# Kernel tuning notes

Hardware: AMD Instinct MI355X
Metric: run time of the kernel (lower is better)

The kernel has to match this reference:

```python
import jax, jax.numpy as jnp
import numpy as np

TOPK = 3  # matches init_kwargs topk


def setup_inputs() -> dict:
    key = jax.random.key(0)
    k1, k2, k3 = jax.random.split(key, 3)
    B, N, D, E, L = 256, 1024, 1024, 8, 1000
    features = jax.random.normal(k1, (B, N, D), dtype=jnp.float32)
    gate_w = jax.random.normal(k2, (D, E), dtype=jnp.float32) * (1.0 / np.sqrt(D))
    gate_b = jnp.zeros((E,), dtype=jnp.float32)
    cls_w = jax.random.normal(k3, (E, L, D), dtype=jnp.float32) * (1.0 / np.sqrt(D))
    cls_b = jnp.zeros((E, L), dtype=jnp.float32)
    return {"features": features, "gate_w": gate_w, "gate_b": gate_b,
            "cls_w": cls_w, "cls_b": cls_b}


def reference(features, gate_w, gate_b, cls_w, cls_b):
    # features: [B, N, D]; gate_w: [D, E]; cls_w: [E, L, D]
    B = features.shape[0]
    E = cls_w.shape[0]
    gate_score = features @ gate_w + gate_b                      # [B, N, E]
    gate_prob = jax.nn.softmax(gate_score.transpose(0, 2, 1), axis=-1)  # [B, E, N] softmax over tokens
    top_v, top_i = jax.lax.top_k(gate_prob, TOPK)                # [B, E, K]
    # gather top-k token features per expert -> [B, E, K, D]
    gathered = features[jnp.arange(B)[:, None, None], top_i]
    comb_w = jax.nn.softmax(top_v, axis=-1)                      # [B, E, K]
    # per-expert linear: [B, E, K, L]
    logits = jnp.einsum('bekd,eld->bekl', gathered, cls_w) + cls_b[None, :, None, :]
    # weighted sum over K, then mean over experts -> [B, L]
    out = jnp.einsum('bekl,bek->bl', logits, comb_w) / E
    return out
```

## Files before the change

kernel.cpp:

```cpp
#include <hip/hip_runtime.h>
#include <hip/hip_bf16.h>
#include <cfloat>

#define B_ 256
#define N_ 1024
#define D_ 1024
#define E_ 8
#define L_ 1000

typedef float f32x4 __attribute__((ext_vector_type(4)));
typedef short bf16x8 __attribute__((ext_vector_type(8)));

__device__ inline unsigned short f2bf(float f) {
  unsigned u = __builtin_bit_cast(unsigned, f);
  u += 0x7fffu + ((u >> 16) & 1u);
  return (unsigned short)(u >> 16);
}

__global__ __launch_bounds__(256) void k_gate(const float* __restrict__ feat,
                                              const float* __restrict__ gate_w,
                                              float* __restrict__ scores) {
  __shared__ float gwT[E_ * D_];
  const int t = threadIdx.x;
#pragma unroll
  for (int j = 0; j < 32; ++j) {
    int idx = j * 256 + t;
    int e = idx & 7, d = idx >> 3;
    gwT[e * D_ + d] = gate_w[idx];
  }
  __syncthreads();

  const int wave = t >> 6, lane = t & 63;
  const long rowBase = ((long)blockIdx.x * 4 + wave) * 8;
  const float* fbase = feat + rowBase * D_;

  float acc[64];
#pragma unroll
  for (int j = 0; j < 64; ++j) acc[j] = 0.f;

#pragma unroll
  for (int it = 0; it < 4; ++it) {
    const int d0 = it * 256 + lane * 4;
    float4 f[8];
#pragma unroll
    for (int r = 0; r < 8; ++r) f[r] = *(const float4*)(fbase + r * D_ + d0);
#pragma unroll
    for (int e = 0; e < 8; ++e) {
      const float4 g = *(const float4*)(&gwT[e * D_ + d0]);
#pragma unroll
      for (int r = 0; r < 8; ++r) {
        acc[r * 8 + e] = fmaf(f[r].x, g.x,
                         fmaf(f[r].y, g.y,
                         fmaf(f[r].z, g.z,
                         fmaf(f[r].w, g.w, acc[r * 8 + e]))));
      }
    }
  }

#pragma unroll
  for (int s = 0; s < 6; ++s) {
    const int m = 1 << s;
    const int half = 32 >> s;
    const bool up = (lane & m) != 0;
#pragma unroll
    for (int j = 0; j < half; ++j) {
      float keep = up ? acc[j + half] : acc[j];
      float send = up ? acc[j] : acc[j + half];
      float recv = __shfl_xor(send, m, 64);
      acc[j] = keep + recv;
    }
  }
  const int idx = ((lane & 1) << 5) | ((lane & 2) << 3) | ((lane & 4) << 1) |
                  ((lane & 8) >> 1) | ((lane & 16) >> 3) | ((lane & 32) >> 5);
  scores[rowBase * 8 + idx] = acc[0];
}

__global__ __launch_bounds__(256) void k_topk(const float* __restrict__ scores,
                                              int* __restrict__ top_i,
                                              float* __restrict__ comb) {
  const int t = threadIdx.x, wave = t >> 6, lane = t & 63;
  const int pair = blockIdx.x * 4 + wave;
  const int b = pair >> 3, e = pair & 7;
  const float* s = scores + (long)b * N_ * E_ + e;

  float v[16];
#pragma unroll
  for (int j = 0; j < 16; ++j) v[j] = s[(j * 64 + lane) * E_];

  float M[3];
  int I[3];
  float Z = 0.f;
#pragma unroll
  for (int k = 0; k < 3; ++k) {
    float lm = -FLT_MAX;
    int ln = 0x7fffffff;
#pragma unroll
    for (int j = 0; j < 16; ++j) {
      if (v[j] > lm) { lm = v[j]; ln = j * 64 + lane; }
    }
#pragma unroll
    for (int s2 = 1; s2 < 64; s2 <<= 1) {
      float om = __shfl_xor(lm, s2, 64);
      int on = __shfl_xor(ln, s2, 64);
      if (om > lm || (om == lm && on < ln)) { lm = om; ln = on; }
    }
    M[k] = lm;
    I[k] = ln;
    if (k == 0) {
      float se = 0.f;
#pragma unroll
      for (int j = 0; j < 16; ++j) se += expf(v[j] - lm);
#pragma unroll
      for (int s2 = 1; s2 < 64; s2 <<= 1) se += __shfl_xor(se, s2, 64);
      Z = se;
    }
    const int slot = ln >> 6, owner = ln & 63;
#pragma unroll
    for (int j = 0; j < 16; ++j)
      if (j == slot && owner == lane) v[j] = -FLT_MAX;
  }

  if (lane == 0) {
    const float p0 = 1.f / Z;
    const float p1 = expf(M[1] - M[0]) / Z;
    const float p2 = expf(M[2] - M[0]) / Z;
    const float c1 = expf(p1 - p0);
    const float c2 = expf(p2 - p0);
    const float den = 1.f + c1 + c2;
    top_i[pair * 3 + 0] = I[0];
    top_i[pair * 3 + 1] = I[1];
    top_i[pair * 3 + 2] = I[2];
    comb[pair * 3 + 0] = 1.f / den;
    comb[pair * 3 + 1] = c1 / den;
    comb[pair * 3 + 2] = c2 / den;
  }
}

__global__ __launch_bounds__(256) void k_gather(const float* __restrict__ feat,
                                                const int* __restrict__ top_i,
                                                const float* __restrict__ comb,
                                                unsigned short* __restrict__ wf) {
  const int pair = blockIdx.x;
  const int b = pair >> 3;
  const int i0 = top_i[pair * 3 + 0];
  const int i1 = top_i[pair * 3 + 1];
  const int i2 = top_i[pair * 3 + 2];
  const float c0 = comb[pair * 3 + 0];
  const float c1 = comb[pair * 3 + 1];
  const float c2 = comb[pair * 3 + 2];
  const float* f = feat + (long)b * N_ * D_;
  const int d = threadIdx.x * 4;
  const float4 x = *(const float4*)(f + (long)i0 * D_ + d);
  const float4 y = *(const float4*)(f + (long)i1 * D_ + d);
  const float4 z = *(const float4*)(f + (long)i2 * D_ + d);
  ushort4 o;
  o.x = f2bf(c0 * x.x + c1 * y.x + c2 * z.x);
  o.y = f2bf(c0 * x.y + c1 * y.y + c2 * z.y);
  o.z = f2bf(c0 * x.z + c1 * y.z + c2 * z.z);
  o.w = f2bf(c0 * x.w + c1 * y.w + c2 * z.w);
  *(ushort4*)(wf + (long)pair * D_ + d) = o;
}

__global__ __launch_bounds__(256) void k_cls(const unsigned short* __restrict__ wf,
                                             const float* __restrict__ cls_w,
                                             float* __restrict__ part) {
  __shared__ uint4 Ag[2][128 * 8];
  __shared__ uint4 Bg[2][64 * 8];

  const int bx = blockIdx.x;
  const int e = bx >> 5, bt = (bx >> 4) & 1, lt = bx & 15;
  const int m0 = bt * 128, l0 = lt * 64;
  const int t = threadIdx.x;
  const int w = t >> 6, lane = t & 63;
  const int wm = w >> 1, wn = w & 1;

  const int arow = t >> 1, ah = t & 1;
  const int brow = t >> 2, bq = t & 3;
  const int lg = (l0 + brow < L_) ? (l0 + brow) : (L_ - 1);
  const unsigned short* agp = wf + ((size_t)(m0 + arow) * E_ + e) * D_ + ah * 32;
  const float* bgp = cls_w + ((size_t)e * L_ + lg) * D_ + bq * 16;

  uint4 areg[4];
  float4 breg[4];

  auto load_regs = [&](int step) {
    const int d0 = step * 64;
#pragma unroll
    for (int j = 0; j < 4; ++j)
      areg[j] = *(const uint4*)(agp + d0 + j * 8);
#pragma unroll
    for (int j = 0; j < 4; ++j)
      breg[j] = *(const float4*)(bgp + d0 + j * 4);
  };

  auto write_lds = [&](int c) {
#pragma unroll
    for (int j = 0; j < 4; ++j)
      Ag[c][arow * 8 + ((ah * 4 + j) ^ (arow & 7))] = areg[j];
#pragma unroll
    for (int j = 0; j < 2; ++j) {
      const float4 x = breg[j * 2], y = breg[j * 2 + 1];
      uint4 p;
      p.x = (unsigned)f2bf(x.x) | ((unsigned)f2bf(x.y) << 16);
      p.y = (unsigned)f2bf(x.z) | ((unsigned)f2bf(x.w) << 16);
      p.z = (unsigned)f2bf(y.x) | ((unsigned)f2bf(y.y) << 16);
      p.w = (unsigned)f2bf(y.z) | ((unsigned)f2bf(y.w) << 16);
      Bg[c][brow * 8 + ((bq * 2 + j) ^ (brow & 7))] = p;
    }
  };

  f32x4 acc[4][2];
#pragma unroll
  for (int m = 0; m < 4; ++m)
#pragma unroll
    for (int n = 0; n < 2; ++n) acc[m][n] = (f32x4){0.f, 0.f, 0.f, 0.f};

  const int l15 = lane & 15, lhi = lane >> 4, l7 = lane & 7;

  load_regs(0);
  for (int step = 0; step < 16; ++step) {
    const int c = step & 1;
    write_lds(c);
    if (step < 15) load_regs(step + 1);
    __syncthreads();
#pragma unroll
    for (int ks = 0; ks < 2; ++ks) {
      bf16x8 a[4], b[2];
#pragma unroll
      for (int m = 0; m < 4; ++m) {
        const int row = wm * 64 + m * 16 + l15;
        a[m] = __builtin_bit_cast(bf16x8,
                 Ag[c][row * 8 + ((ks * 4 + lhi) ^ l7)]);
      }
#pragma unroll
      for (int n = 0; n < 2; ++n) {
        const int row = wn * 32 + n * 16 + l15;
        b[n] = __builtin_bit_cast(bf16x8,
                 Bg[c][row * 8 + ((ks * 4 + lhi) ^ l7)]);
      }
#pragma unroll
      for (int m = 0; m < 4; ++m)
#pragma unroll
        for (int n = 0; n < 2; ++n)
          acc[m][n] = __builtin_amdgcn_mfma_f32_16x16x32_bf16(
              a[m], b[n], acc[m][n], 0, 0, 0);
    }
    __syncthreads();
  }

#pragma unroll
  for (int m = 0; m < 4; ++m) {
#pragma unroll
    for (int n = 0; n < 2; ++n) {
      const int col = l0 + wn * 32 + n * 16 + l15;
      if (col < L_) {
#pragma unroll
        for (int j = 0; j < 4; ++j) {
          const int row = m0 + wm * 64 + m * 16 + lhi * 4 + j;
          part[((size_t)e * B_ + row) * L_ + col] = acc[m][n][j];
        }
      }
    }
  }
}

__global__ __launch_bounds__(256) void k_reduce(const float* __restrict__ part,
                                                const float* __restrict__ cls_b,
                                                float* __restrict__ out) {
  const int idx = blockIdx.x * 256 + threadIdx.x;
  if (idx >= B_ * L_) return;
  const int l = idx % L_;
  float s = 0.f, bias = 0.f;
#pragma unroll
  for (int e = 0; e < 8; ++e) {
    s += part[(long)e * (B_ * L_) + idx];
    bias += cls_b[e * L_ + l];
  }
  out[idx] = (s + bias) * 0.125f;
}

extern "C" void kernel_launch(void* const* d_in, const int* in_sizes, int n_in,
                              void* d_out, int out_size, void* d_ws, size_t ws_size,
                              hipStream_t stream) {
  const float* feat   = (const float*)d_in[0];
  const float* gate_w = (const float*)d_in[1];
  const float* cls_w  = (const float*)d_in[3];
  const float* cls_b  = (const float*)d_in[4];
  float* out = (float*)d_out;

  char* ws = (char*)d_ws;
  float*          scores = (float*)ws;
  float*          part   = (float*)ws;
  unsigned short* wfb    = (unsigned short*)(ws + 8388608);
  int*            top_i  = (int*)(ws + 16777216);
  float*          comb   = (float*)(ws + 16801792);

  k_gate<<<8192, 256, 0, stream>>>(feat, gate_w, scores);
  k_topk<<<512, 256, 0, stream>>>(scores, top_i, comb);
  k_gather<<<2048, 256, 0, stream>>>(feat, top_i, comb, wfb);
  k_cls<<<256, 256, 0, stream>>>(wfb, cls_w, part);
  k_reduce<<<1000, 256, 0, stream>>>(part, cls_b, out);
}
```

Baseline: 241.4 us.

## Fuse top-k with gather, transpose gate scores, and halve classifier M tile

The gate kernel now stages its scores through shared memory and writes them expert-major, so each (batch, expert) score row is contiguous and top-k can read it with float4 loads instead of stride-8 loads. Top-k and the weighted gather are fused into one kernel: wave 0 picks the indices and weights, then shares them with the block via LDS. This drops a launch and the top_i/comb round trip through global memory. The classifier GEMM tile shrinks from 128 to 64 rows, doubling the grid to 512 blocks for better CU occupancy, at the cost of reading the cls_w tiles twice as often.

```diff
diff --git a/kernel.cpp b/kernel.cpp
--- a/kernel.cpp
+++ b/kernel.cpp
@@ -21,6 +21,7 @@
                                               const float* __restrict__ gate_w,
                                               float* __restrict__ scores) {
   __shared__ float gwT[E_ * D_];
+  __shared__ float sm[8][132];
   const int t = threadIdx.x;
 #pragma unroll
   for (int j = 0; j < 32; ++j) {
@@ -72,122 +73,124 @@
   }
   const int idx = ((lane & 1) << 5) | ((lane & 2) << 3) | ((lane & 4) << 1) |
                   ((lane & 8) >> 1) | ((lane & 16) >> 3) | ((lane & 32) >> 5);
-  scores[rowBase * 8 + idx] = acc[0];
-}
-
-__global__ __launch_bounds__(256) void k_topk(const float* __restrict__ scores,
-                                              int* __restrict__ top_i,
-                                              float* __restrict__ comb) {
-  const int t = threadIdx.x, wave = t >> 6, lane = t & 63;
-  const int pair = blockIdx.x * 4 + wave;
+  sm[idx & 7][wave * 8 + (idx >> 3)] = acc[0];
+  __syncthreads();
+  const int te = t >> 5, tr = t & 31;
+  scores[(size_t)te * (B_ * N_) + (long)blockIdx.x * 32 + tr] = sm[te][tr];
+}
+
+__global__ __launch_bounds__(256) void k_topk_gather(
+    const float* __restrict__ scores, const float* __restrict__ feat,
+    unsigned short* __restrict__ wf) {
+  __shared__ int sI[3];
+  __shared__ float sC[3];
+  const int t = threadIdx.x, w = t >> 6, lane = t & 63;
+  const int pair = blockIdx.x;
   const int b = pair >> 3, e = pair & 7;
-  const float* s = scores + (long)b * N_ * E_ + e;
-
-  float v[16];
-#pragma unroll
-  for (int j = 0; j < 16; ++j) v[j] = s[(j * 64 + lane) * E_];
-
-  float M[3];
-  int I[3];
-  float Z = 0.f;
-#pragma unroll
-  for (int k = 0; k < 3; ++k) {
-    float lm = -FLT_MAX;
-    int ln = 0x7fffffff;
-#pragma unroll
-    for (int j = 0; j < 16; ++j) {
-      if (v[j] > lm) { lm = v[j]; ln = j * 64 + lane; }
-    }
-#pragma unroll
-    for (int s2 = 1; s2 < 64; s2 <<= 1) {
-      float om = __shfl_xor(lm, s2, 64);
-      int on = __shfl_xor(ln, s2, 64);
-      if (om > lm || (om == lm && on < ln)) { lm = om; ln = on; }
-    }
-    M[k] = lm;
-    I[k] = ln;
-    if (k == 0) {
-      float se = 0.f;
-#pragma unroll
-      for (int j = 0; j < 16; ++j) se += expf(v[j] - lm);
-#pragma unroll
-      for (int s2 = 1; s2 < 64; s2 <<= 1) se += __shfl_xor(se, s2, 64);
-      Z = se;
-    }
-    const int slot = ln >> 6, owner = ln & 63;
-#pragma unroll
-    for (int j = 0; j < 16; ++j)
-      if (j == slot && owner == lane) v[j] = -FLT_MAX;
-  }
-
-  if (lane == 0) {
-    const float p0 = 1.f / Z;
-    const float p1 = expf(M[1] - M[0]) / Z;
-    const float p2 = expf(M[2] - M[0]) / Z;
-    const float c1 = expf(p1 - p0);
-    const float c2 = expf(p2 - p0);
-    const float den = 1.f + c1 + c2;
-    top_i[pair * 3 + 0] = I[0];
-    top_i[pair * 3 + 1] = I[1];
-    top_i[pair * 3 + 2] = I[2];
-    comb[pair * 3 + 0] = 1.f / den;
-    comb[pair * 3 + 1] = c1 / den;
-    comb[pair * 3 + 2] = c2 / den;
-  }
-}
-
-__global__ __launch_bounds__(256) void k_gather(const float* __restrict__ feat,
-                                                const int* __restrict__ top_i,
-                                                const float* __restrict__ comb,
-                                                unsigned short* __restrict__ wf) {
-  const int pair = blockIdx.x;
-  const int b = pair >> 3;
-  const int i0 = top_i[pair * 3 + 0];
-  const int i1 = top_i[pair * 3 + 1];
-  const int i2 = top_i[pair * 3 + 2];
-  const float c0 = comb[pair * 3 + 0];
-  const float c1 = comb[pair * 3 + 1];
-  const float c2 = comb[pair * 3 + 2];
-  const float* f = feat + (long)b * N_ * D_;
-  const int d = threadIdx.x * 4;
-  const float4 x = *(const float4*)(f + (long)i0 * D_ + d);
-  const float4 y = *(const float4*)(f + (long)i1 * D_ + d);
-  const float4 z = *(const float4*)(f + (long)i2 * D_ + d);
+
+  if (w == 0) {
+    const float* s = scores + (size_t)e * (B_ * N_) + (size_t)b * N_;
+    float v[16];
+#pragma unroll
+    for (int j = 0; j < 4; ++j) {
+      const float4 x = *(const float4*)(s + j * 256 + lane * 4);
+      v[j * 4 + 0] = x.x; v[j * 4 + 1] = x.y;
+      v[j * 4 + 2] = x.z; v[j * 4 + 3] = x.w;
+    }
+
+    float M[3];
+    int I[3];
+    float Z = 0.f;
+#pragma unroll
+    for (int k = 0; k < 3; ++k) {
+      float lm = -FLT_MAX;
+      int ln = 0x7fffffff;
+#pragma unroll
+      for (int j = 0; j < 4; ++j)
+#pragma unroll
+        for (int c = 0; c < 4; ++c) {
+          const float val = v[j * 4 + c];
+          if (val > lm) { lm = val; ln = j * 256 + lane * 4 + c; }
+        }
+#pragma unroll
+      for (int s2 = 1; s2 < 64; s2 <<= 1) {
+        float om = __shfl_xor(lm, s2, 64);
+        int on = __shfl_xor(ln, s2, 64);
+        if (om > lm || (om == lm && on < ln)) { lm = om; ln = on; }
+      }
+      M[k] = lm;
+      I[k] = ln;
+      if (k == 0) {
+        float se = 0.f;
+#pragma unroll
+        for (int j = 0; j < 16; ++j) se += expf(v[j] - lm);
+#pragma unroll
+        for (int s2 = 1; s2 < 64; s2 <<= 1) se += __shfl_xor(se, s2, 64);
+        Z = se;
+      }
+      const int slot = ln >> 8, owner = (ln >> 2) & 63, comp = ln & 3;
+#pragma unroll
+      for (int j = 0; j < 4; ++j)
+#pragma unroll
+        for (int c = 0; c < 4; ++c)
+          if (j == slot && c == comp && owner == lane)
+            v[j * 4 + c] = -FLT_MAX;
+    }
+
+    if (lane == 0) {
+      const float p0 = 1.f / Z;
+      const float p1 = expf(M[1] - M[0]) / Z;
+      const float p2 = expf(M[2] - M[0]) / Z;
+      const float c1 = expf(p1 - p0);
+      const float c2 = expf(p2 - p0);
+      const float den = 1.f + c1 + c2;
+      sI[0] = I[0]; sI[1] = I[1]; sI[2] = I[2];
+      sC[0] = 1.f / den; sC[1] = c1 / den; sC[2] = c2 / den;
+    }
+  }
+  __syncthreads();
+
+  const int i0 = sI[0], i1 = sI[1], i2 = sI[2];
+  const float c0 = sC[0], c1 = sC[1], c2 = sC[2];
+  const float* f = feat + (size_t)b * N_ * D_;
+  const int d = t * 4;
+  const float4 x = *(const float4*)(f + (size_t)i0 * D_ + d);
+  const float4 y = *(const float4*)(f + (size_t)i1 * D_ + d);
+  const float4 z = *(const float4*)(f + (size_t)i2 * D_ + d);
   ushort4 o;
   o.x = f2bf(c0 * x.x + c1 * y.x + c2 * z.x);
   o.y = f2bf(c0 * x.y + c1 * y.y + c2 * z.y);
   o.z = f2bf(c0 * x.z + c1 * y.z + c2 * z.z);
   o.w = f2bf(c0 * x.w + c1 * y.w + c2 * z.w);
-  *(ushort4*)(wf + (long)pair * D_ + d) = o;
+  *(ushort4*)(wf + (size_t)pair * D_ + d) = o;
 }
 
 __global__ __launch_bounds__(256) void k_cls(const unsigned short* __restrict__ wf,
                                              const float* __restrict__ cls_w,
                                              float* __restrict__ part) {
-  __shared__ uint4 Ag[2][128 * 8];
+  __shared__ uint4 Ag[2][64 * 8];
   __shared__ uint4 Bg[2][64 * 8];
 
   const int bx = blockIdx.x;
-  const int e = bx >> 5, bt = (bx >> 4) & 1, lt = bx & 15;
-  const int m0 = bt * 128, l0 = lt * 64;
+  const int e = bx >> 6, lt = (bx >> 2) & 15, bt = bx & 3;
+  const int m0 = bt * 64, l0 = lt * 64;
   const int t = threadIdx.x;
   const int w = t >> 6, lane = t & 63;
   const int wm = w >> 1, wn = w & 1;
 
-  const int arow = t >> 1, ah = t & 1;
-  const int brow = t >> 2, bq = t & 3;
-  const int lg = (l0 + brow < L_) ? (l0 + brow) : (L_ - 1);
-  const unsigned short* agp = wf + ((size_t)(m0 + arow) * E_ + e) * D_ + ah * 32;
+  const int ar = t >> 2, ag2 = t & 3;
+  const int br = t >> 2, bq = t & 3;
+  const int lg = (l0 + br < L_) ? (l0 + br) : (L_ - 1);
+  const unsigned short* agp = wf + ((size_t)(m0 + ar) * E_ + e) * D_ + ag2 * 16;
   const float* bgp = cls_w + ((size_t)e * L_ + lg) * D_ + bq * 16;
 
-  uint4 areg[4];
+  uint4 areg[2];
   float4 breg[4];
 
   auto load_regs = [&](int step) {
     const int d0 = step * 64;
-#pragma unroll
-    for (int j = 0; j < 4; ++j)
-      areg[j] = *(const uint4*)(agp + d0 + j * 8);
+    areg[0] = *(const uint4*)(agp + d0);
+    areg[1] = *(const uint4*)(agp + d0 + 8);
 #pragma unroll
     for (int j = 0; j < 4; ++j)
       breg[j] = *(const float4*)(bgp + d0 + j * 4);
@@ -195,8 +198,8 @@
 
   auto write_lds = [&](int c) {
 #pragma unroll
-    for (int j = 0; j < 4; ++j)
-      Ag[c][arow * 8 + ((ah * 4 + j) ^ (arow & 7))] = areg[j];
+    for (int j = 0; j < 2; ++j)
+      Ag[c][ar * 8 + ((ag2 * 2 + j) ^ (ar & 7))] = areg[j];
 #pragma unroll
     for (int j = 0; j < 2; ++j) {
       const float4 x = breg[j * 2], y = breg[j * 2 + 1];
@@ -205,17 +208,17 @@
       p.y = (unsigned)f2bf(x.z) | ((unsigned)f2bf(x.w) << 16);
       p.z = (unsigned)f2bf(y.x) | ((unsigned)f2bf(y.y) << 16);
       p.w = (unsigned)f2bf(y.z) | ((unsigned)f2bf(y.w) << 16);
-      Bg[c][brow * 8 + ((bq * 2 + j) ^ (brow & 7))] = p;
+      Bg[c][br * 8 + ((bq * 2 + j) ^ (br & 7))] = p;
     }
   };
 
-  f32x4 acc[4][2];
-#pragma unroll
-  for (int m = 0; m < 4; ++m)
+  f32x4 acc[2][2];
+#pragma unroll
+  for (int m = 0; m < 2; ++m)
 #pragma unroll
     for (int n = 0; n < 2; ++n) acc[m][n] = (f32x4){0.f, 0.f, 0.f, 0.f};
 
-  const int l15 = lane & 15, lhi = lane >> 4, l7 = lane & 7;
+  const int l15 = lane & 15, lhi = lane >> 4;
 
   load_regs(0);
   for (int step = 0; step < 16; ++step) {
@@ -225,21 +228,21 @@
     __syncthreads();
 #pragma unroll
     for (int ks = 0; ks < 2; ++ks) {
-      bf16x8 a[4], b[2];
-#pragma unroll
-      for (int m = 0; m < 4; ++m) {
-        const int row = wm * 64 + m * 16 + l15;
+      bf16x8 a[2], b[2];
+#pragma unroll
+      for (int m = 0; m < 2; ++m) {
+        const int row = wm * 32 + m * 16 + l15;
         a[m] = __builtin_bit_cast(bf16x8,
-                 Ag[c][row * 8 + ((ks * 4 + lhi) ^ l7)]);
+                 Ag[c][row * 8 + ((ks * 4 + lhi) ^ (row & 7))]);
       }
 #pragma unroll
       for (int n = 0; n < 2; ++n) {
         const int row = wn * 32 + n * 16 + l15;
         b[n] = __builtin_bit_cast(bf16x8,
-                 Bg[c][row * 8 + ((ks * 4 + lhi) ^ l7)]);
-      }
-#pragma unroll
-      for (int m = 0; m < 4; ++m)
+                 Bg[c][row * 8 + ((ks * 4 + lhi) ^ (row & 7))]);
+      }
+#pragma unroll
+      for (int m = 0; m < 2; ++m)
 #pragma unroll
         for (int n = 0; n < 2; ++n)
           acc[m][n] = __builtin_amdgcn_mfma_f32_16x16x32_bf16(
@@ -249,14 +252,14 @@
   }
 
 #pragma unroll
-  for (int m = 0; m < 4; ++m) {
+  for (int m = 0; m < 2; ++m) {
 #pragma unroll
     for (int n = 0; n < 2; ++n) {
       const int col = l0 + wn * 32 + n * 16 + l15;
       if (col < L_) {
 #pragma unroll
         for (int j = 0; j < 4; ++j) {
-          const int row = m0 + wm * 64 + m * 16 + lhi * 4 + j;
+          const int row = m0 + wm * 32 + m * 16 + lhi * 4 + j;
           part[((size_t)e * B_ + row) * L_ + col] = acc[m][n][j];
         }
       }
@@ -292,12 +295,9 @@
   float*          scores = (float*)ws;
   float*          part   = (float*)ws;
   unsigned short* wfb    = (unsigned short*)(ws + 8388608);
-  int*            top_i  = (int*)(ws + 16777216);
-  float*          comb   = (float*)(ws + 16801792);
 
   k_gate<<<8192, 256, 0, stream>>>(feat, gate_w, scores);
-  k_topk<<<512, 256, 0, stream>>>(scores, top_i, comb);
-  k_gather<<<2048, 256, 0, stream>>>(feat, top_i, comb, wfb);
-  k_cls<<<256, 256, 0, stream>>>(wfb, cls_w, part);
+  k_topk_gather<<<2048, 256, 0, stream>>>(scores, feat, wfb);
+  k_cls<<<512, 256, 0, stream>>>(wfb, cls_w, part);
   k_reduce<<<1000, 256, 0, stream>>>(part, cls_b, out);
 }
```

Result: slower. 249.9 us (+3.5%).
